# Kernel optimization log

Measured on AMD Instinct MI355X. Metric: run time of the kernel, lower is better.

## Reference

```python
import jax, jax.numpy as jnp
import numpy as np

# --- model dims ---
N = 360        # nodes
B = 8          # batch
T = 7500       # hidden_steps = tr/dt = 750/0.1
RATIO = 10     # dt_ratio = dtt/dt
HEMO = T // RATIO
INPUT = 2
DMAX = 500

# --- FastDMFParams defaults ---
DT = 0.1
SQRT_DT = DT ** 0.5
DTT_S = 1.0 / 1000.0            # dtt / 1000 (seconds)
W_E, W_I, I_0 = 1.0, 0.7, 0.382
TAU_E, TAU_I = 100.0, 10.0
GAMMA_E, GAMMA_I = 0.641 / 1000.0, 1.0 / 1000.0
SIGMA_E, SIGMA_I = 0.005, 0.005
AE, BE, DE = 310.0, 125.0, 0.16
AI, BI, DI = 615.0, 177.0, 0.087
G, JN = 2.0, 0.15
G_EE = 1.4
ITAU_S, ITAU_F, ITAU_0 = 1.0 / 0.65, 1.0 / 0.41, 1.0 / 0.98
IALPHA, RHO = 1.0 / 0.32, 0.34
K1, K2, K3 = 2.38, 2.0, 0.48
V0 = 0.2


def setup_inputs() -> dict:
    key = jax.random.key(0)
    k1, k2, k3, k4 = jax.random.split(key, 4)
    baseline = jnp.array([0.0, 0.0, 0.0, 1.0, 1.0, 1.0], jnp.float32).reshape(1, 6, 1)
    state = 0.45 * jax.random.uniform(k1, (N, 6, B), jnp.float32) + baseline
    delays = jnp.zeros((N, DMAX, B), jnp.float32)  # unused (use_delay_based=False)
    noise_in = jax.random.normal(k2, (N, T, INPUT, B), jnp.float32)
    noise_out = jax.random.normal(k3, (N, B), jnp.float32)
    sc = jax.random.uniform(k4, (B, N, N), jnp.float32) / N  # normalized structural connectivity
    return {"state": state, "delays": delays, "noise_in": noise_in,
            "noise_out": noise_out, "sc": sc}


def _firing_rate(a, b, d, cur):
    x = a * cur - b
    return x / (1.0 - jnp.exp(-d * x) + 1e-8)


def _simulate(state, noise_in, noise_out, sc):
    E, I = state[:, 0, :], state[:, 1, :]          # (N,B)
    s, f = state[:, 2, :], state[:, 3, :]
    v, q = state[:, 4, :], state[:, 5, :]

    # inhibitory gain (non-scalar branch): Ji = 1 + 0.75*g*rowsum(sc), (N,B)
    Ji = (1.0 + 0.75 * G * jnp.sum(sc, axis=-1)).T

    # (N,T,INPUT,B) -> (HEMO, RATIO, N, INPUT, B)
    noise = jnp.transpose(noise_in, (1, 0, 2, 3)).reshape(HEMO, RATIO, N, INPUT, B)

    def neural_step(carry, nz):
        E, I = carry
        En, In = nz[:, 0, :], nz[:, 1, :]
        conn = jnp.einsum('bnm,mb->nb', sc, E)                 # delayed-coupling surrogate
        I_E = jax.nn.relu(W_E * I_0 + G_EE * JN * E + G * JN * conn - Ji * I)
        I_I = jax.nn.relu(W_I * I_0 + JN * E - I)
        R_E = _firing_rate(AE, BE, DE, I_E)
        R_I = _firing_rate(AI, BI, DI, I_I)
        dE = -E / TAU_E + (1.0 - E) * GAMMA_E * R_E
        dI = -I / TAU_I + GAMMA_I * R_I
        E = jax.nn.relu(E + DT * dE + SIGMA_E * En * SQRT_DT)
        I = jax.nn.relu(I + DT * dI + SIGMA_I * In * SQRT_DT)
        return (E, I), None

    def hemo_step(carry, noise_block):
        E, I, s, f, v, q = carry
        (E, I), _ = jax.lax.scan(neural_step, (E, I), noise_block)
        # Balloon-Windkessel Euler step at dtt (seconds)
        v_ia = v ** IALPHA
        ds = E - ITAU_S * s - ITAU_F * (f - 1.0)
        df = s
        dv = (f - v_ia) * ITAU_0
        dq = (f / RHO * (1.0 - (1.0 - RHO) ** (1.0 / f)) - q * v_ia / v) * ITAU_0
        s = s + DTT_S * ds
        f = f + DTT_S * df
        v = v + DTT_S * dv
        q = q + DTT_S * dq
        return (E, I, s, f, v, q), None

    (E, I, s, f, v, q), _ = jax.lax.scan(hemo_step, (E, I, s, f, v, q), noise)
    bold = 100.0 * V0 * (K1 * (1.0 - q) + K2 * (1.0 - q / v) + K3 * (1.0 - v)) + noise_out
    next_state = jnp.stack([E, I, s, f, v, q], axis=1)  # (N,6,B)
    return next_state, bold


def reference(state, delays, noise_in, noise_out, sc):
    # delays buffer unused (params.use_delay_based = False)
    return _simulate(state, noise_in, noise_out, sc)
```

## Files before the change

kernel.cpp:

```cpp
#include <hip/hip_runtime.h>


typedef unsigned int u32;
typedef uint4 u32x4;

#define NN 360
#define NB 8
#define NT 7500
#define NHEMO 750

#define S_SC 45720.0f
#define S_E  64.0f
#define CONN_K 1.0252653e-7f

#if __has_builtin(__builtin_amdgcn_sdot4)
#define DOT4(a,b,c) __builtin_amdgcn_sdot4((a),(b),(c),false)
#elif __has_builtin(__builtin_amdgcn_udot4)
#define DOT4(a,b,c) (int)__builtin_amdgcn_udot4((u32)(a),(u32)(b),(u32)(c),false)
#else
static __device__ __forceinline__ int DOT4(int a, int b, int c) {
  #pragma unroll
  for (int i = 0; i < 4; ++i) c += ((a >> (8*i)) & 0xff) * ((b >> (8*i)) & 0xff);
  return c;
}
#endif

__device__ __forceinline__ float frcp(float x) {
#if __has_builtin(__builtin_amdgcn_rcpf)
  return __builtin_amdgcn_rcpf(x);
#else
  return 1.0f / x;
#endif
}
__device__ __forceinline__ float fexp2(float x) {
#if __has_builtin(__builtin_amdgcn_exp2f)
  return __builtin_amdgcn_exp2f(x);
#else
  return exp2f(x);
#endif
}
__device__ __forceinline__ float flog2(float x) {
#if __has_builtin(__builtin_amdgcn_logf)
  return __builtin_amdgcn_logf(x);
#else
  return log2f(x);
#endif
}

template <int CTRL>
__device__ __forceinline__ int dpp_add_i(int x) {
  return x + __builtin_amdgcn_mov_dpp(x, CTRL, 0xF, 0xF, true);
}
template <int CTRL>
__device__ __forceinline__ float dpp_add_f(float x) {
  return x + __int_as_float(__builtin_amdgcn_mov_dpp(__float_as_int(x), CTRL, 0xF, 0xF, true));
}

__global__ __launch_bounds__(512, 2) void dmf_kernel(
    const float* __restrict__ state,
    const float* __restrict__ noise_in,
    const float* __restrict__ noise_out,
    const float* __restrict__ sc,
    float* __restrict__ out)
{
  const int b   = blockIdx.x;
  const int tid = threadIdx.x;
  const int w   = tid >> 6;
  const int l   = tid & 63;
  const int cg  = l & 3;
  const int rg  = l >> 2;

  const bool upd = (cg < 3) && (rg < 15);
  const int lrow = 3*rg + cg;
  const int urow = 45*w + lrow;

  __shared__ u32 Eq[2][96];

  if (tid < 192) ((u32*)Eq)[tid] = 0;

  int scp[3][24];
  float rs[3] = {0.f, 0.f, 0.f};
  const int c0 = 90 * cg;
  #pragma unroll
  for (int j = 0; j < 3; ++j) {
    const int rr = 3*rg + j;
    const bool rvalid = (rr < 45);
    const float* sp = sc + ((size_t)b*NN + (45*w + rr))*NN;
    #pragma unroll
    for (int k = 0; k < 24; ++k) {
      int pack = 0;
      #pragma unroll
      for (int e = 0; e < 4; ++e) {
        const int cc = 4*k + e;
        int q = 0;
        if (rvalid && cc < 90) {
          const float x = sp[c0 + cc];
          rs[j] += x;
          q = (int)rintf(x * S_SC);
        }
        pack |= q << (8*e);
      }
      scp[j][k] = pack;
    }
  }

  #pragma unroll
  for (int j = 0; j < 3; ++j) {
    rs[j] = dpp_add_f<0xB1>(rs[j]);
    rs[j] = dpp_add_f<0x4E>(rs[j]);
  }
  const float rsum = (cg == 0) ? rs[0] : ((cg == 1) ? rs[1] : rs[2]);

  float E=0.f, I=0.f, ss=0.f, ff=0.f, vv=0.f, qq=0.f, Ji=0.f;
  const float* np = noise_in + (size_t)urow * NT * 2 * NB + b;
  float n0E=0.f, n0I=0.f, n1E=0.f, n1I=0.f;
  int boff = 0;
  __syncthreads();
  if (upd) {
    Ji = 1.0f + 1.5f * rsum;
    const float* st = state + (size_t)urow * 6 * NB + b;
    E  = st[0];
    I  = st[NB];
    ss = st[2*NB];
    ff = st[3*NB];
    vv = st[4*NB];
    qq = st[5*NB];
    const int ch = urow / 90;
    boff = urow + 6*ch;
    int q = (int)rintf(E * S_E);
    q = q > 127 ? 127 : q;
    ((char*)&Eq[0][0])[boff] = (char)q;
    n0E = np[0];      n0I = np[NB];
    n1E = np[2*NB];   n1I = np[3*NB];
  }
  np += 4*NB;
  __syncthreads();

  const u32x4* eq0 = (const u32x4*)&Eq[0][24*cg];
  const u32x4* eq1 = (const u32x4*)&Eq[1][24*cg];
  char* pb0 = (char*)&Eq[0][0] + boff;
  char* pb1 = (char*)&Eq[1][0] + boff;

  auto body = [&](const u32x4* cur, char* nxt, bool PF, bool hemo) {
    u32x4 ev[6];
    #pragma unroll
    for (int kk = 0; kk < 6; ++kk) ev[kk] = cur[kk];

    float n2E = n1E, n2I = n1I;
    if (PF) {
      if (upd) { n2E = np[0]; n2I = np[NB]; }
      np += 2*NB;
    }

    int a0 = 0, a1 = 0, a2 = 0;
    #pragma unroll
    for (int kk = 0; kk < 6; ++kk) {
      const u32x4 e = ev[kk];
      a0 = DOT4(scp[0][4*kk+0], (int)e.x, a0);
      a1 = DOT4(scp[1][4*kk+0], (int)e.x, a1);
      a2 = DOT4(scp[2][4*kk+0], (int)e.x, a2);
      a0 = DOT4(scp[0][4*kk+1], (int)e.y, a0);
      a1 = DOT4(scp[1][4*kk+1], (int)e.y, a1);
      a2 = DOT4(scp[2][4*kk+1], (int)e.y, a2);
      a0 = DOT4(scp[0][4*kk+2], (int)e.z, a0);
      a1 = DOT4(scp[1][4*kk+2], (int)e.z, a1);
      a2 = DOT4(scp[2][4*kk+2], (int)e.z, a2);
      a0 = DOT4(scp[0][4*kk+3], (int)e.w, a0);
      a1 = DOT4(scp[1][4*kk+3], (int)e.w, a1);
      a2 = DOT4(scp[2][4*kk+3], (int)e.w, a2);
    }
    a0 = dpp_add_i<0xB1>(a0); a0 = dpp_add_i<0x4E>(a0);
    a1 = dpp_add_i<0xB1>(a1); a1 = dpp_add_i<0x4E>(a1);
    a2 = dpp_add_i<0xB1>(a2); a2 = dpp_add_i<0x4E>(a2);
    const int ci = (cg == 0) ? a0 : ((cg == 1) ? a1 : a2);

    if (upd) {
      const float cs = (float)ci * CONN_K;
      float I_E = fmaxf(0.382f + 0.21f*E + cs - Ji*I, 0.f);
      float I_I = fmaxf(0.2674f + 0.15f*E - I, 0.f);
      const float xE  = 310.f*I_E - 125.f;
      const float R_E = xE * frcp(1.f - __expf(-0.16f*xE) + 1e-8f);
      const float xI  = 615.f*I_I - 177.f;
      const float R_I = xI * frcp(1.f - __expf(-0.087f*xI) + 1e-8f);
      const float dE = -E*0.01f + (1.f - E)*0.000641f*R_E;
      const float dI = -I*0.1f  + 0.001f*R_I;
      E = fmaxf(E + 0.1f*dE + 0.00158113883f*n0E, 0.f);
      I = fmaxf(I + 0.1f*dI + 0.00158113883f*n0I, 0.f);
      int q = (int)rintf(E * S_E);
      q = q > 127 ? 127 : q;
      *nxt = (char)q;
      if (hemo) {
        const float l2v  = flog2(vv);
        const float v_ia = fexp2(3.125f * l2v);
        const float v_r  = fexp2(2.125f * l2v);
        const float ds_  = E - 1.53846153846f*ss - 2.43902439024f*(ff - 1.f);
        const float df_  = ss;
        const float dv_  = (ff - v_ia) * 1.02040816327f;
        const float pw   = fexp2(-0.59946207f * frcp(ff));
        const float dq_  = (ff*2.94117647059f*(1.f - pw) - qq*v_r) * 1.02040816327f;
        ss += 1e-3f*ds_;
        ff += 1e-3f*df_;
        vv += 1e-3f*dv_;
        qq += 1e-3f*dq_;
      }
    }
    n0E = n1E; n0I = n1I;
    n1E = n2E; n1I = n2I;
    __syncthreads();
  };

  for (int hs = 0; hs < NHEMO; ++hs) {
    body(eq0, pb1, true, false);
    body(eq1, pb0, true, false);
    body(eq0, pb1, true, false);
    body(eq1, pb0, true, false);
    body(eq0, pb1, true, false);
    body(eq1, pb0, true, false);
    body(eq0, pb1, true, false);
    body(eq1, pb0, true, false);
    if (hs != NHEMO - 1) {
      body(eq0, pb1, true, false);
      body(eq1, pb0, true, true);
    } else {
      body(eq0, pb1, false, false);
      body(eq1, pb0, false, true);
    }
  }

  if (upd) {
    float* o = out + (size_t)urow * 6 * NB + b;
    o[0]    = E;
    o[NB]   = I;
    o[2*NB] = ss;
    o[3*NB] = ff;
    o[4*NB] = vv;
    o[5*NB] = qq;
    out[NN*6*NB + urow*NB + b] =
        20.f*(2.38f*(1.f - qq) + 2.f*(1.f - qq/vv) + 0.48f*(1.f - vv))
        + noise_out[urow*NB + b];
  }
}

extern "C" void kernel_launch(void* const* d_in, const int* in_sizes, int n_in,
                              void* d_out, int out_size, void* d_ws, size_t ws_size,
                              hipStream_t stream) {
  const float* state     = (const float*)d_in[0];
  const float* noise_in  = (const float*)d_in[2];
  const float* noise_out = (const float*)d_in[3];
  const float* sc        = (const float*)d_in[4];
  float* out = (float*)d_out;
  dmf_kernel<<<NB, 512, 0, stream>>>(state, noise_in, noise_out, sc, out);
}
```

Baseline: 4.676 ms.

## Repartition matvec to 8-lane column groups with 6 rows and packed-float update

Work is remapped so each 8-lane group covers 6 rows, with each lane owning 48 columns. Per step this loads 3 LDS vectors instead of 6, and the E buffer is laid out contiguously without padding. The E/I update is written with 2-wide float vectors and exp2 with folded constants. The barrier becomes a hand-rolled s_waitcnt plus s_barrier with scheduling fences. The catch is an extra DPP reduction stage and more idle lanes, since 2 of every 8 do no update.

```diff
diff --git a/kernel.cpp b/kernel.cpp
--- a/kernel.cpp
+++ b/kernel.cpp
@@ -3,6 +3,7 @@
 
 typedef unsigned int u32;
 typedef uint4 u32x4;
+typedef float f32x2 __attribute__((ext_vector_type(2)));
 
 #define NN 360
 #define NB 8
@@ -54,6 +55,14 @@
 template <int CTRL>
 __device__ __forceinline__ float dpp_add_f(float x) {
   return x + __int_as_float(__builtin_amdgcn_mov_dpp(__float_as_int(x), CTRL, 0xF, 0xF, true));
+}
+
+__device__ __forceinline__ void lds_barrier() {
+  __builtin_amdgcn_sched_barrier(0);
+  asm volatile("s_waitcnt lgkmcnt(0)" ::: "memory");
+  __builtin_amdgcn_s_barrier();
+  asm volatile("" ::: "memory");
+  __builtin_amdgcn_sched_barrier(0);
 }
 
 __global__ __launch_bounds__(512, 2) void dmf_kernel(
@@ -67,133 +76,161 @@
   const int tid = threadIdx.x;
   const int w   = tid >> 6;
   const int l   = tid & 63;
-  const int cg  = l & 3;
-  const int rg  = l >> 2;
-
-  const bool upd = (cg < 3) && (rg < 15);
-  const int lrow = 3*rg + cg;
-  const int urow = 45*w + lrow;
+  const int sl  = l & 7;
+  const int oc  = l >> 3;
+
+  const int rbase = 48*w + 6*oc;
+  const int urow  = rbase + sl;
+  const bool upd  = (sl < 6) && (urow < NN);
+  const int jj    = (sl < 3) ? sl : sl - 3;
 
   __shared__ u32 Eq[2][96];
 
   if (tid < 192) ((u32*)Eq)[tid] = 0;
 
-  int scp[3][24];
-  float rs[3] = {0.f, 0.f, 0.f};
-  const int c0 = 90 * cg;
+  int scp[6][12];
+  float rs[6];
+  const int c0 = 48 * sl;
   #pragma unroll
-  for (int j = 0; j < 3; ++j) {
-    const int rr = 3*rg + j;
-    const bool rvalid = (rr < 45);
-    const float* sp = sc + ((size_t)b*NN + (45*w + rr))*NN;
-    #pragma unroll
-    for (int k = 0; k < 24; ++k) {
+  for (int j = 0; j < 6; ++j) {
+    const int gr = rbase + j;
+    const bool rvalid = (gr < NN);
+    const float* sp = sc + ((size_t)b*NN + (rvalid ? gr : 0))*NN;
+    float rsj = 0.f;
+    #pragma unroll
+    for (int k = 0; k < 12; ++k) {
       int pack = 0;
       #pragma unroll
       for (int e = 0; e < 4; ++e) {
-        const int cc = 4*k + e;
+        const int cc = c0 + 4*k + e;
         int q = 0;
-        if (rvalid && cc < 90) {
-          const float x = sp[c0 + cc];
-          rs[j] += x;
+        if (rvalid && cc < NN) {
+          const float x = sp[cc];
+          rsj += x;
           q = (int)rintf(x * S_SC);
         }
         pack |= q << (8*e);
       }
       scp[j][k] = pack;
     }
+    rs[j] = rsj;
   }
 
   #pragma unroll
-  for (int j = 0; j < 3; ++j) {
+  for (int j = 0; j < 6; ++j) {
     rs[j] = dpp_add_f<0xB1>(rs[j]);
     rs[j] = dpp_add_f<0x4E>(rs[j]);
-  }
-  const float rsum = (cg == 0) ? rs[0] : ((cg == 1) ? rs[1] : rs[2]);
-
-  float E=0.f, I=0.f, ss=0.f, ff=0.f, vv=0.f, qq=0.f, Ji=0.f;
+    rs[j] = dpp_add_f<0x141>(rs[j]);
+  }
+  const float mfA = (sl < 3) ? rs[0] : rs[3];
+  const float mfB = (sl < 3) ? rs[1] : rs[4];
+  const float mfC = (sl < 3) ? rs[2] : rs[5];
+  const float rsum = (jj == 0) ? mfA : ((jj == 1) ? mfB : mfC);
+
+  f32x2 EI = {0.f, 0.f};
+  float ss=0.f, ff=0.f, vv=0.f, qq=0.f, Ji=0.f;
   const float* np = noise_in + (size_t)urow * NT * 2 * NB + b;
-  float n0E=0.f, n0I=0.f, n1E=0.f, n1I=0.f;
-  int boff = 0;
+  f32x2 n0 = {0.f, 0.f}, n1 = {0.f, 0.f};
   __syncthreads();
   if (upd) {
     Ji = 1.0f + 1.5f * rsum;
     const float* st = state + (size_t)urow * 6 * NB + b;
-    E  = st[0];
-    I  = st[NB];
+    EI.x = st[0];
+    EI.y = st[NB];
     ss = st[2*NB];
     ff = st[3*NB];
     vv = st[4*NB];
     qq = st[5*NB];
-    const int ch = urow / 90;
-    boff = urow + 6*ch;
-    int q = (int)rintf(E * S_E);
+    int q = (int)rintf(EI.x * S_E);
     q = q > 127 ? 127 : q;
-    ((char*)&Eq[0][0])[boff] = (char)q;
-    n0E = np[0];      n0I = np[NB];
-    n1E = np[2*NB];   n1I = np[3*NB];
+    ((char*)&Eq[0][0])[urow] = (char)q;
+    n0.x = np[0];      n0.y = np[NB];
+    n1.x = np[2*NB];   n1.y = np[3*NB];
   }
   np += 4*NB;
   __syncthreads();
 
-  const u32x4* eq0 = (const u32x4*)&Eq[0][24*cg];
-  const u32x4* eq1 = (const u32x4*)&Eq[1][24*cg];
-  char* pb0 = (char*)&Eq[0][0] + boff;
-  char* pb1 = (char*)&Eq[1][0] + boff;
+  const u32x4* eq0 = (const u32x4*)&Eq[0][12*sl];
+  const u32x4* eq1 = (const u32x4*)&Eq[1][12*sl];
+  char* pb0 = (char*)&Eq[0][0] + urow;
+  char* pb1 = (char*)&Eq[1][0] + urow;
 
   auto body = [&](const u32x4* cur, char* nxt, bool PF, bool hemo) {
-    u32x4 ev[6];
-    #pragma unroll
-    for (int kk = 0; kk < 6; ++kk) ev[kk] = cur[kk];
-
-    float n2E = n1E, n2I = n1I;
+    const u32x4 e0 = cur[0];
+    const u32x4 e1 = cur[1];
+    const u32x4 e2 = cur[2];
+
+    f32x2 n2 = n1;
     if (PF) {
-      if (upd) { n2E = np[0]; n2I = np[NB]; }
+      if (upd) { n2.x = np[0]; n2.y = np[NB]; }
       np += 2*NB;
     }
 
-    int a0 = 0, a1 = 0, a2 = 0;
-    #pragma unroll
-    for (int kk = 0; kk < 6; ++kk) {
-      const u32x4 e = ev[kk];
-      a0 = DOT4(scp[0][4*kk+0], (int)e.x, a0);
-      a1 = DOT4(scp[1][4*kk+0], (int)e.x, a1);
-      a2 = DOT4(scp[2][4*kk+0], (int)e.x, a2);
-      a0 = DOT4(scp[0][4*kk+1], (int)e.y, a0);
-      a1 = DOT4(scp[1][4*kk+1], (int)e.y, a1);
-      a2 = DOT4(scp[2][4*kk+1], (int)e.y, a2);
-      a0 = DOT4(scp[0][4*kk+2], (int)e.z, a0);
-      a1 = DOT4(scp[1][4*kk+2], (int)e.z, a1);
-      a2 = DOT4(scp[2][4*kk+2], (int)e.z, a2);
-      a0 = DOT4(scp[0][4*kk+3], (int)e.w, a0);
-      a1 = DOT4(scp[1][4*kk+3], (int)e.w, a1);
-      a2 = DOT4(scp[2][4*kk+3], (int)e.w, a2);
-    }
-    a0 = dpp_add_i<0xB1>(a0); a0 = dpp_add_i<0x4E>(a0);
-    a1 = dpp_add_i<0xB1>(a1); a1 = dpp_add_i<0x4E>(a1);
-    a2 = dpp_add_i<0xB1>(a2); a2 = dpp_add_i<0x4E>(a2);
-    const int ci = (cg == 0) ? a0 : ((cg == 1) ? a1 : a2);
+    int a0=0, a1=0, a2=0, a3=0, a4=0, a5=0;
+    #pragma unroll
+    for (int q4 = 0; q4 < 4; ++q4) {
+      const int ex = (q4==0) ? (int)e0.x : (q4==1) ? (int)e0.y : (q4==2) ? (int)e0.z : (int)e0.w;
+      a0 = DOT4(scp[0][q4], ex, a0);
+      a1 = DOT4(scp[1][q4], ex, a1);
+      a2 = DOT4(scp[2][q4], ex, a2);
+      a3 = DOT4(scp[3][q4], ex, a3);
+      a4 = DOT4(scp[4][q4], ex, a4);
+      a5 = DOT4(scp[5][q4], ex, a5);
+    }
+    #pragma unroll
+    for (int q4 = 0; q4 < 4; ++q4) {
+      const int ex = (q4==0) ? (int)e1.x : (q4==1) ? (int)e1.y : (q4==2) ? (int)e1.z : (int)e1.w;
+      a0 = DOT4(scp[0][4+q4], ex, a0);
+      a1 = DOT4(scp[1][4+q4], ex, a1);
+      a2 = DOT4(scp[2][4+q4], ex, a2);
+      a3 = DOT4(scp[3][4+q4], ex, a3);
+      a4 = DOT4(scp[4][4+q4], ex, a4);
+      a5 = DOT4(scp[5][4+q4], ex, a5);
+    }
+    #pragma unroll
+    for (int q4 = 0; q4 < 4; ++q4) {
+      const int ex = (q4==0) ? (int)e2.x : (q4==1) ? (int)e2.y : (q4==2) ? (int)e2.z : (int)e2.w;
+      a0 = DOT4(scp[0][8+q4], ex, a0);
+      a1 = DOT4(scp[1][8+q4], ex, a1);
+      a2 = DOT4(scp[2][8+q4], ex, a2);
+      a3 = DOT4(scp[3][8+q4], ex, a3);
+      a4 = DOT4(scp[4][8+q4], ex, a4);
+      a5 = DOT4(scp[5][8+q4], ex, a5);
+    }
+    a0 = dpp_add_i<0xB1>(a0); a0 = dpp_add_i<0x4E>(a0); a0 = dpp_add_i<0x141>(a0);
+    a1 = dpp_add_i<0xB1>(a1); a1 = dpp_add_i<0x4E>(a1); a1 = dpp_add_i<0x141>(a1);
+    a2 = dpp_add_i<0xB1>(a2); a2 = dpp_add_i<0x4E>(a2); a2 = dpp_add_i<0x141>(a2);
+    a3 = dpp_add_i<0xB1>(a3); a3 = dpp_add_i<0x4E>(a3); a3 = dpp_add_i<0x141>(a3);
+    a4 = dpp_add_i<0xB1>(a4); a4 = dpp_add_i<0x4E>(a4); a4 = dpp_add_i<0x141>(a4);
+    a5 = dpp_add_i<0xB1>(a5); a5 = dpp_add_i<0x4E>(a5); a5 = dpp_add_i<0x141>(a5);
+    const int mA = (sl < 3) ? a0 : a3;
+    const int mB = (sl < 3) ? a1 : a4;
+    const int mC = (sl < 3) ? a2 : a5;
+    const int ci = (jj == 0) ? mA : ((jj == 1) ? mB : mC);
 
     if (upd) {
-      const float cs = (float)ci * CONN_K;
-      float I_E = fmaxf(0.382f + 0.21f*E + cs - Ji*I, 0.f);
-      float I_I = fmaxf(0.2674f + 0.15f*E - I, 0.f);
-      const float xE  = 310.f*I_E - 125.f;
-      const float R_E = xE * frcp(1.f - __expf(-0.16f*xE) + 1e-8f);
-      const float xI  = 615.f*I_I - 177.f;
-      const float R_I = xI * frcp(1.f - __expf(-0.087f*xI) + 1e-8f);
-      const float dE = -E*0.01f + (1.f - E)*0.000641f*R_E;
-      const float dI = -I*0.1f  + 0.001f*R_I;
-      E = fmaxf(E + 0.1f*dE + 0.00158113883f*n0E, 0.f);
-      I = fmaxf(I + 0.1f*dI + 0.00158113883f*n0I, 0.f);
-      int q = (int)rintf(E * S_E);
+      const float conn = (float)ci * CONN_K;
+      f32x2 P;
+      P.x = 0.382f + 0.21f*EI.x + conn - Ji*EI.y;
+      P.y = 0.2674f + 0.15f*EI.x - EI.y;
+      P = P > (f32x2){0.f, 0.f} ? P : (f32x2){0.f, 0.f};
+      f32x2 X = P * (f32x2){310.f, 615.f} + (f32x2){-125.f, -177.f};
+      f32x2 Ax = X * (f32x2){-0.23083120f, -0.12551447f};
+      f32x2 Ex = {fexp2(Ax.x), fexp2(Ax.y)};
+      f32x2 Dn = (f32x2){1.00000001f, 1.00000001f} - Ex;
+      f32x2 Rr = X * (f32x2){frcp(Dn.x), frcp(Dn.y)};
+      f32x2 Gg = {(1.f - EI.x) * 0.000641f, 0.001f};
+      f32x2 Dd = Gg * Rr + EI * (f32x2){-0.01f, -0.1f};
+      EI = EI + Dd * (f32x2){0.1f, 0.1f} + n0 * (f32x2){0.00158113883f, 0.00158113883f};
+      EI = EI > (f32x2){0.f, 0.f} ? EI : (f32x2){0.f, 0.f};
+      int q = (int)(EI.x * S_E + 0.5f);
       q = q > 127 ? 127 : q;
       *nxt = (char)q;
       if (hemo) {
         const float l2v  = flog2(vv);
         const float v_ia = fexp2(3.125f * l2v);
         const float v_r  = fexp2(2.125f * l2v);
-        const float ds_  = E - 1.53846153846f*ss - 2.43902439024f*(ff - 1.f);
+        const float ds_  = EI.x - 1.53846153846f*ss - 2.43902439024f*(ff - 1.f);
         const float df_  = ss;
         const float dv_  = (ff - v_ia) * 1.02040816327f;
         const float pw   = fexp2(-0.59946207f * frcp(ff));
@@ -204,9 +241,8 @@
         qq += 1e-3f*dq_;
       }
     }
-    n0E = n1E; n0I = n1I;
-    n1E = n2E; n1I = n2I;
-    __syncthreads();
+    n0 = n1; n1 = n2;
+    lds_barrier();
   };
 
   for (int hs = 0; hs < NHEMO; ++hs) {
@@ -229,8 +265,8 @@
 
   if (upd) {
     float* o = out + (size_t)urow * 6 * NB + b;
-    o[0]    = E;
-    o[NB]   = I;
+    o[0]    = EI.x;
+    o[NB]   = EI.y;
     o[2*NB] = ss;
     o[3*NB] = ff;
     o[4*NB] = vv;
```

Result: slower. 7.112 ms (+52.1%).

## Compute int8 coupling matvec with MFMA 16x16x64 instead of sdot4 chains

Applied to the files above, without the earlier changes.

Swaps the per-lane packed int8 sdot4 dot products and DPP reductions for MFMA i32_16x16x64_i8 instructions. SC rows are laid out as A fragments and the quantized E vector is broadcast as the B operand. Row ownership is remapped to the MFMA output layout and the syncthreads is replaced by a manual lgkmcnt wait plus s_barrier. It also uses exp2 directly and replaces rintf with add-and-truncate. The MFMA does redundant work, since only one output column is useful, and the serial latency of the dependent MFMA chain sits on a latency-bound per-step critical path.

```diff
diff --git a/kernel.cpp b/kernel.cpp
--- a/kernel.cpp
+++ b/kernel.cpp
@@ -2,7 +2,7 @@
 
 
 typedef unsigned int u32;
-typedef uint4 u32x4;
+typedef int i32x4 __attribute__((ext_vector_type(4)));
 
 #define NN 360
 #define NB 8
@@ -12,18 +12,6 @@
 #define S_SC 45720.0f
 #define S_E  64.0f
 #define CONN_K 1.0252653e-7f
-
-#if __has_builtin(__builtin_amdgcn_sdot4)
-#define DOT4(a,b,c) __builtin_amdgcn_sdot4((a),(b),(c),false)
-#elif __has_builtin(__builtin_amdgcn_udot4)
-#define DOT4(a,b,c) (int)__builtin_amdgcn_udot4((u32)(a),(u32)(b),(u32)(c),false)
-#else
-static __device__ __forceinline__ int DOT4(int a, int b, int c) {
-  #pragma unroll
-  for (int i = 0; i < 4; ++i) c += ((a >> (8*i)) & 0xff) * ((b >> (8*i)) & 0xff);
-  return c;
-}
-#endif
 
 __device__ __forceinline__ float frcp(float x) {
 #if __has_builtin(__builtin_amdgcn_rcpf)
@@ -47,13 +35,12 @@
 #endif
 }
 
-template <int CTRL>
-__device__ __forceinline__ int dpp_add_i(int x) {
-  return x + __builtin_amdgcn_mov_dpp(x, CTRL, 0xF, 0xF, true);
-}
-template <int CTRL>
-__device__ __forceinline__ float dpp_add_f(float x) {
-  return x + __int_as_float(__builtin_amdgcn_mov_dpp(__float_as_int(x), CTRL, 0xF, 0xF, true));
+__device__ __forceinline__ void lds_barrier() {
+  __builtin_amdgcn_sched_barrier(0);
+  asm volatile("s_waitcnt lgkmcnt(0)" ::: "memory");
+  __builtin_amdgcn_s_barrier();
+  asm volatile("" ::: "memory");
+  __builtin_amdgcn_sched_barrier(0);
 }
 
 __global__ __launch_bounds__(512, 2) void dmf_kernel(
@@ -67,84 +54,92 @@
   const int tid = threadIdx.x;
   const int w   = tid >> 6;
   const int l   = tid & 63;
-  const int cg  = l & 3;
-  const int rg  = l >> 2;
-
-  const bool upd = (cg < 3) && (rg < 15);
-  const int lrow = 3*rg + cg;
-  const int urow = 45*w + lrow;
-
-  __shared__ u32 Eq[2][96];
-
-  if (tid < 192) ((u32*)Eq)[tid] = 0;
-
-  int scp[3][24];
-  float rs[3] = {0.f, 0.f, 0.f};
-  const int c0 = 90 * cg;
+  const int g   = l >> 4;
+  const int r   = l & 15;
+  const int t_o = r >> 2;
+  const int j_o = r & 3;
+  const int R_o = 48*w + 16*t_o + 4*g + j_o;
+  const bool upd = (r < 12) && (R_o < NN);
+  const int Rn  = upd ? R_o : 0;
+
+  __shared__ u32 xq[2][96];
+
+  if (tid < 192) ((u32*)xq)[tid] = 0;
+
+  i32x4 afr[3][6];
+  float rs[3];
   #pragma unroll
-  for (int j = 0; j < 3; ++j) {
-    const int rr = 3*rg + j;
-    const bool rvalid = (rr < 45);
-    const float* sp = sc + ((size_t)b*NN + (45*w + rr))*NN;
-    #pragma unroll
-    for (int k = 0; k < 24; ++k) {
-      int pack = 0;
+  for (int t = 0; t < 3; ++t) {
+    const int R = 48*w + 16*t + r;
+    const bool rv = (R < NN);
+    const float* sp = sc + ((size_t)b*NN + (rv ? R : 0))*NN;
+    float acc = 0.f;
+    #pragma unroll
+    for (int kf = 0; kf < 6; ++kf) {
+      i32x4 pk;
       #pragma unroll
-      for (int e = 0; e < 4; ++e) {
-        const int cc = 4*k + e;
-        int q = 0;
-        if (rvalid && cc < 90) {
-          const float x = sp[c0 + cc];
-          rs[j] += x;
-          q = (int)rintf(x * S_SC);
+      for (int d = 0; d < 4; ++d) {
+        int packv = 0;
+        #pragma unroll
+        for (int e = 0; e < 4; ++e) {
+          const int k = 64*kf + 16*g + 4*d + e;
+          int q = 0;
+          if (rv && k < NN) {
+            const float x = sp[k];
+            acc += x;
+            q = (int)rintf(x * S_SC);
+          }
+          packv |= q << (8*e);
         }
-        pack |= q << (8*e);
+        pk[d] = packv;
       }
-      scp[j][k] = pack;
-    }
-  }
-
+      afr[t][kf] = pk;
+    }
+    rs[t] = acc;
+  }
   #pragma unroll
-  for (int j = 0; j < 3; ++j) {
-    rs[j] = dpp_add_f<0xB1>(rs[j]);
-    rs[j] = dpp_add_f<0x4E>(rs[j]);
-  }
-  const float rsum = (cg == 0) ? rs[0] : ((cg == 1) ? rs[1] : rs[2]);
+  for (int t = 0; t < 3; ++t) {
+    rs[t] += __shfl_xor(rs[t], 16, 64);
+    rs[t] += __shfl_xor(rs[t], 32, 64);
+  }
+  const int rho = 4*g + j_o;
+  const int qs0 = __builtin_amdgcn_ds_bpermute(4*rho, __float_as_int(rs[0]));
+  const int qs1 = __builtin_amdgcn_ds_bpermute(4*rho, __float_as_int(rs[1]));
+  const int qs2 = __builtin_amdgcn_ds_bpermute(4*rho, __float_as_int(rs[2]));
+  const float rsum = __int_as_float((t_o == 0) ? qs0 : ((t_o == 1) ? qs1 : qs2));
 
   float E=0.f, I=0.f, ss=0.f, ff=0.f, vv=0.f, qq=0.f, Ji=0.f;
-  const float* np = noise_in + (size_t)urow * NT * 2 * NB + b;
+  const float* np = noise_in + (size_t)Rn * NT * 2 * NB + b;
   float n0E=0.f, n0I=0.f, n1E=0.f, n1I=0.f;
-  int boff = 0;
   __syncthreads();
   if (upd) {
     Ji = 1.0f + 1.5f * rsum;
-    const float* st = state + (size_t)urow * 6 * NB + b;
+    const float* st = state + (size_t)R_o * 6 * NB + b;
     E  = st[0];
     I  = st[NB];
     ss = st[2*NB];
     ff = st[3*NB];
     vv = st[4*NB];
     qq = st[5*NB];
-    const int ch = urow / 90;
-    boff = urow + 6*ch;
-    int q = (int)rintf(E * S_E);
-    q = q > 127 ? 127 : q;
-    ((char*)&Eq[0][0])[boff] = (char)q;
+    int qv = (int)rintf(E * S_E);
+    qv = qv > 127 ? 127 : qv;
+    ((char*)&xq[0][0])[R_o] = (char)qv;
     n0E = np[0];      n0I = np[NB];
     n1E = np[2*NB];   n1I = np[3*NB];
   }
   np += 4*NB;
   __syncthreads();
 
-  const u32x4* eq0 = (const u32x4*)&Eq[0][24*cg];
-  const u32x4* eq1 = (const u32x4*)&Eq[1][24*cg];
-  char* pb0 = (char*)&Eq[0][0] + boff;
-  char* pb1 = (char*)&Eq[1][0] + boff;
-
-  auto body = [&](const u32x4* cur, char* nxt, bool PF, bool hemo) {
-    u32x4 ev[6];
-    #pragma unroll
-    for (int kk = 0; kk < 6; ++kk) ev[kk] = cur[kk];
+  const u32* xb0 = &xq[0][4*g];
+  const u32* xb1 = &xq[1][4*g];
+  char* pb0 = (char*)&xq[0][0] + Rn;
+  char* pb1 = (char*)&xq[1][0] + Rn;
+  const bool w7 = (w == 7);
+
+  auto body = [&](const u32* xb, char* pbn, bool PF, bool hemo) {
+    i32x4 bf[6];
+    #pragma unroll
+    for (int kf = 0; kf < 6; ++kf) bf[kf] = *(const i32x4*)(xb + 16*kf);
 
     float n2E = n1E, n2I = n1I;
     if (PF) {
@@ -152,43 +147,37 @@
       np += 2*NB;
     }
 
-    int a0 = 0, a1 = 0, a2 = 0;
-    #pragma unroll
-    for (int kk = 0; kk < 6; ++kk) {
-      const u32x4 e = ev[kk];
-      a0 = DOT4(scp[0][4*kk+0], (int)e.x, a0);
-      a1 = DOT4(scp[1][4*kk+0], (int)e.x, a1);
-      a2 = DOT4(scp[2][4*kk+0], (int)e.x, a2);
-      a0 = DOT4(scp[0][4*kk+1], (int)e.y, a0);
-      a1 = DOT4(scp[1][4*kk+1], (int)e.y, a1);
-      a2 = DOT4(scp[2][4*kk+1], (int)e.y, a2);
-      a0 = DOT4(scp[0][4*kk+2], (int)e.z, a0);
-      a1 = DOT4(scp[1][4*kk+2], (int)e.z, a1);
-      a2 = DOT4(scp[2][4*kk+2], (int)e.z, a2);
-      a0 = DOT4(scp[0][4*kk+3], (int)e.w, a0);
-      a1 = DOT4(scp[1][4*kk+3], (int)e.w, a1);
-      a2 = DOT4(scp[2][4*kk+3], (int)e.w, a2);
-    }
-    a0 = dpp_add_i<0xB1>(a0); a0 = dpp_add_i<0x4E>(a0);
-    a1 = dpp_add_i<0xB1>(a1); a1 = dpp_add_i<0x4E>(a1);
-    a2 = dpp_add_i<0xB1>(a2); a2 = dpp_add_i<0x4E>(a2);
-    const int ci = (cg == 0) ? a0 : ((cg == 1) ? a1 : a2);
+    i32x4 ac0 = {0,0,0,0}, ac1 = {0,0,0,0}, ac2 = {0,0,0,0};
+    #pragma unroll
+    for (int kf = 0; kf < 6; ++kf)
+      ac0 = __builtin_amdgcn_mfma_i32_16x16x64_i8(afr[0][kf], bf[kf], ac0, 0, 0, 0);
+    #pragma unroll
+    for (int kf = 0; kf < 6; ++kf)
+      ac1 = __builtin_amdgcn_mfma_i32_16x16x64_i8(afr[1][kf], bf[kf], ac1, 0, 0, 0);
+    if (!w7) {
+      #pragma unroll
+      for (int kf = 0; kf < 6; ++kf)
+        ac2 = __builtin_amdgcn_mfma_i32_16x16x64_i8(afr[2][kf], bf[kf], ac2, 0, 0, 0);
+    }
+
+    const i32x4 at = (t_o == 0) ? ac0 : ((t_o == 1) ? ac1 : ac2);
+    const int ci = (j_o == 0) ? at.x : ((j_o == 1) ? at.y : ((j_o == 2) ? at.z : at.w));
 
     if (upd) {
       const float cs = (float)ci * CONN_K;
       float I_E = fmaxf(0.382f + 0.21f*E + cs - Ji*I, 0.f);
       float I_I = fmaxf(0.2674f + 0.15f*E - I, 0.f);
       const float xE  = 310.f*I_E - 125.f;
-      const float R_E = xE * frcp(1.f - __expf(-0.16f*xE) + 1e-8f);
+      const float R_E = xE * frcp(1.f - fexp2(-0.23083120f*xE) + 1e-8f);
       const float xI  = 615.f*I_I - 177.f;
-      const float R_I = xI * frcp(1.f - __expf(-0.087f*xI) + 1e-8f);
+      const float R_I = xI * frcp(1.f - fexp2(-0.12551447f*xI) + 1e-8f);
       const float dE = -E*0.01f + (1.f - E)*0.000641f*R_E;
       const float dI = -I*0.1f  + 0.001f*R_I;
       E = fmaxf(E + 0.1f*dE + 0.00158113883f*n0E, 0.f);
       I = fmaxf(I + 0.1f*dI + 0.00158113883f*n0I, 0.f);
-      int q = (int)rintf(E * S_E);
-      q = q > 127 ? 127 : q;
-      *nxt = (char)q;
+      int qv = (int)(E * S_E + 0.5f);
+      qv = qv > 127 ? 127 : qv;
+      *pbn = (char)qv;
       if (hemo) {
         const float l2v  = flog2(vv);
         const float v_ia = fexp2(3.125f * l2v);
@@ -206,38 +195,38 @@
     }
     n0E = n1E; n0I = n1I;
     n1E = n2E; n1I = n2I;
-    __syncthreads();
+    lds_barrier();
   };
 
   for (int hs = 0; hs < NHEMO; ++hs) {
-    body(eq0, pb1, true, false);
-    body(eq1, pb0, true, false);
-    body(eq0, pb1, true, false);
-    body(eq1, pb0, true, false);
-    body(eq0, pb1, true, false);
-    body(eq1, pb0, true, false);
-    body(eq0, pb1, true, false);
-    body(eq1, pb0, true, false);
+    body(xb0, pb1, true, false);
+    body(xb1, pb0, true, false);
+    body(xb0, pb1, true, false);
+    body(xb1, pb0, true, false);
+    body(xb0, pb1, true, false);
+    body(xb1, pb0, true, false);
+    body(xb0, pb1, true, false);
+    body(xb1, pb0, true, false);
     if (hs != NHEMO - 1) {
-      body(eq0, pb1, true, false);
-      body(eq1, pb0, true, true);
+      body(xb0, pb1, true, false);
+      body(xb1, pb0, true, true);
     } else {
-      body(eq0, pb1, false, false);
-      body(eq1, pb0, false, true);
+      body(xb0, pb1, false, false);
+      body(xb1, pb0, false, true);
     }
   }
 
   if (upd) {
-    float* o = out + (size_t)urow * 6 * NB + b;
+    float* o = out + (size_t)R_o * 6 * NB + b;
     o[0]    = E;
     o[NB]   = I;
     o[2*NB] = ss;
     o[3*NB] = ff;
     o[4*NB] = vv;
     o[5*NB] = qq;
-    out[NN*6*NB + urow*NB + b] =
+    out[NN*6*NB + R_o*NB + b] =
         20.f*(2.38f*(1.f - qq) + 2.f*(1.f - qq/vv) + 0.48f*(1.f - vv))
-        + noise_out[urow*NB + b];
+        + noise_out[R_o*NB + b];
   }
 }
 
```

Result: faster. 4.388 ms (median of 2 runs) (-6.2%).
